# Kernel optimization log

Measured on AMD Instinct MI355X. Metric: run time of the kernel, lower is better.

Reference implementation:

```python
import jax, jax.numpy as jnp
import numpy as np

N_HEADS = 16
HEAD_DIM = 64


def apply_rope(x, cos, sin):
    # x: [B, H, S, D]; cos/sin: [S, D//2]
    x_even = x[..., ::2]
    x_odd = x[..., 1::2]
    c = cos[None, None, :, :]
    s = sin[None, None, :, :]
    rot_even = x_even * c - x_odd * s
    rot_odd = x_even * s + x_odd * c
    return jnp.stack((rot_even, rot_odd), axis=-1).reshape(x.shape)


def setup_inputs() -> dict:
    key = jax.random.key(0)
    ks = jax.random.split(key, 7)
    B, S, D = 2, 2048, 1024
    x = jax.random.normal(ks[0], (B, S, D), dtype=jnp.float32)
    # realistic rope tables
    inv_freq = 1.0 / (10000.0 ** (np.arange(0, HEAD_DIM, 2, dtype=np.float32) / HEAD_DIM))
    t = np.arange(S, dtype=np.float32)
    freqs = np.outer(t, inv_freq)  # [S, HEAD_DIM//2]
    rope_cos = jnp.asarray(np.cos(freqs), dtype=jnp.float32)
    rope_sin = jnp.asarray(np.sin(freqs), dtype=jnp.float32)
    Wqkv = jax.random.normal(ks[1], (D, 3 * D), dtype=jnp.float32) * (D ** -0.5)
    bqkv = jax.random.normal(ks[2], (3 * D,), dtype=jnp.float32) * 0.02
    Wout = jax.random.normal(ks[3], (D, D), dtype=jnp.float32) * (D ** -0.5)
    bout = jax.random.normal(ks[4], (D,), dtype=jnp.float32) * 0.02
    return {"x": x, "rope_cos": rope_cos, "rope_sin": rope_sin,
            "Wqkv": Wqkv, "bqkv": bqkv, "Wout": Wout, "bout": bout}


def reference(x, rope_cos, rope_sin, Wqkv, bqkv, Wout, bout):
    B, S, D = x.shape
    H, Hd = N_HEADS, HEAD_DIM
    qkv = x @ Wqkv + bqkv                      # [B, S, 3D]
    qkv = qkv.reshape(B, S, 3, H, Hd).transpose(2, 0, 3, 1, 4)  # [3, B, H, S, Hd]
    q, k, v = qkv[0], qkv[1], qkv[2]
    q = apply_rope(q, rope_cos, rope_sin)
    k = apply_rope(k, rope_cos, rope_sin)
    scale = Hd ** -0.5
    scores = jnp.einsum('bhqd,bhkd->bhqk', q, k) * scale
    causal = jnp.tril(jnp.ones((S, S), dtype=bool))
    scores = jnp.where(causal[None, None], scores, jnp.finfo(scores.dtype).min)
    attn = jax.nn.softmax(scores, axis=-1)
    out = jnp.einsum('bhqk,bhkd->bhqd', attn, v)  # [B, H, S, Hd]
    out = out.transpose(0, 2, 1, 3).reshape(B, S, D)
    return out @ Wout + bout
```

## Files before the change

### kernel.cpp

```cpp
#include <hip/hip_runtime.h>
#include <hip/hip_bf16.h>

typedef unsigned short u16;
typedef __attribute__((ext_vector_type(4))) float f32x4;
typedef __attribute__((ext_vector_type(16))) float f32x16;
typedef __attribute__((ext_vector_type(8))) short short8;
typedef __attribute__((ext_vector_type(8))) unsigned short ushort8;

#define AS1 __attribute__((address_space(1)))
#define AS3 __attribute__((address_space(3)))

__device__ __forceinline__ u16 f2bf(float f) {
  union { float f; unsigned u; } v; v.f = f;
  unsigned r = v.u + 0x7fffu + ((v.u >> 16) & 1u);
  return (u16)(r >> 16);
}
__device__ __forceinline__ float b2f(u16 h) {
  union { unsigned u; float f; } v; v.u = ((unsigned)h) << 16;
  return v.f;
}
__device__ __forceinline__ f32x4 mfma16(short8 a, short8 b, f32x4 c) {
  return __builtin_amdgcn_mfma_f32_16x16x32_bf16(a, b, c, 0, 0, 0);
}
__device__ __forceinline__ f32x16 mfma32(short8 a, short8 b, f32x16 c) {
  return __builtin_amdgcn_mfma_f32_32x32x16_bf16(a, b, c, 0, 0, 0);
}
__device__ __forceinline__ unsigned cvtpk(float a, float b) {
  unsigned r;
  asm("v_cvt_pk_bf16_f32 %0, %1, %2" : "=v"(r) : "v"(a), "v"(b));
  return r;
}
__device__ __forceinline__ short8 pack4(unsigned w0, unsigned w1, unsigned w2, unsigned w3) {
  union { unsigned u[4]; short8 s; } t;
  t.u[0] = w0; t.u[1] = w1; t.u[2] = w2; t.u[3] = w3;
  return t.s;
}
__device__ __forceinline__ float exp2h(float x) { return __builtin_amdgcn_exp2f(x); }

__global__ __launch_bounds__(256) void cvt_f32_bf16_k(const float* __restrict__ in,
                                                      u16* __restrict__ out, int n8) {
  int t = blockIdx.x * 256 + threadIdx.x;
  if (t >= n8) return;
  const float4* p = (const float4*)(in + (size_t)t * 8);
  float4 a = p[0], b = p[1];
  ushort8 o;
  o[0] = f2bf(a.x); o[1] = f2bf(a.y); o[2] = f2bf(a.z); o[3] = f2bf(a.w);
  o[4] = f2bf(b.x); o[5] = f2bf(b.y); o[6] = f2bf(b.z); o[7] = f2bf(b.w);
  *(ushort8*)(out + (size_t)t * 8) = o;
}

__global__ __launch_bounds__(256) void transpose_f32_bf16_k(const float* __restrict__ in,
                                                            u16* __restrict__ out, int R, int C) {
  __shared__ float tile[32][33];
  int bc = blockIdx.x * 32, br = blockIdx.y * 32;
  int tx = threadIdx.x & 31, ty = threadIdx.x >> 5;
#pragma unroll
  for (int p = 0; p < 4; ++p)
    tile[ty + p * 8][tx] = in[(size_t)(br + ty + p * 8) * C + bc + tx];
  __syncthreads();
#pragma unroll
  for (int p = 0; p < 4; ++p)
    out[(size_t)(bc + ty + p * 8) * R + br + tx] = f2bf(tile[tx][ty + p * 8]);
}

__global__ __launch_bounds__(256, 6) void gemm_n64_k(const u16* __restrict__ A,
                                                     const u16* __restrict__ Bt,
                                                     const float* __restrict__ bias,
                                                     const float* __restrict__ cosT,
                                                     const float* __restrict__ sinT,
                                                     u16* __restrict__ Cout) {
  __shared__ __align__(16) u16 As[128 * 32];
  __shared__ __align__(16) u16 Bs[64 * 32];
  const int tid = threadIdx.x, lane = tid & 63, w = tid >> 6;
  const int g = lane >> 4, c16 = lane & 15;
  const int rowBase = blockIdx.y * 128, colBase = blockIdx.x * 64;
  f32x4 acc[2][4] = {};
  const int e0 = (w * 2 + 0) * 512 + lane * 8;
  const int e1 = (w * 2 + 1) * 512 + lane * 8;
  const u16* Ag0 = A + (size_t)(rowBase + (e0 >> 5)) * 1024 + (e0 & 31);
  const u16* Ag1 = A + (size_t)(rowBase + (e1 >> 5)) * 1024 + (e1 & 31);
  const u16* Bg0 = Bt + (size_t)(colBase + (tid >> 2)) * 1024 + (tid & 3) * 8;
  u16* As0 = As + (w * 2 + 0) * 512;
  u16* As1 = As + (w * 2 + 1) * 512;
  u16* Bs0 = Bs + w * 512;

  for (int k0 = 0; k0 < 1024; k0 += 32) {
    __builtin_amdgcn_global_load_lds((const AS1 void*)(Ag0 + k0), (AS3 void*)As0, 16, 0, 0);
    __builtin_amdgcn_global_load_lds((const AS1 void*)(Ag1 + k0), (AS3 void*)As1, 16, 0, 0);
    __builtin_amdgcn_global_load_lds((const AS1 void*)(Bg0 + k0), (AS3 void*)Bs0, 16, 0, 0);
    asm volatile("s_waitcnt vmcnt(0)" ::: "memory");
    __syncthreads();
    short8 af[2], bfr[4];
#pragma unroll
    for (int i = 0; i < 2; ++i)
      af[i] = *(const short8*)(As + ((w * 32 + i * 16 + c16) * 32 + g * 8));
#pragma unroll
    for (int j = 0; j < 4; ++j)
      bfr[j] = *(const short8*)(Bs + ((j * 16 + c16) * 32 + g * 8));
#pragma unroll
    for (int i = 0; i < 2; ++i)
#pragma unroll
      for (int j = 0; j < 4; ++j) acc[i][j] = mfma16(af[i], bfr[j], acc[i][j]);
    __syncthreads();
  }

#pragma unroll
  for (int i = 0; i < 2; ++i) {
    int mbase = rowBase + w * 32 + i * 16 + 4 * g;
#pragma unroll
    for (int j = 0; j < 4; ++j) {
      int n = colBase + j * 16 + c16;
      float bv = bias[n];
      const int which = n >> 10, hh = (n >> 6) & 15, d = n & 63;
#pragma unroll
      for (int r = 0; r < 4; ++r) {
        float v = acc[i][j][r] + bv;
        int m = mbase + r;
        int bb = m >> 11, s = m & 2047;
        float outv = v;
        if (which < 2) {
          float pv = __shfl_xor(v, 1);
          float cc = cosT[(size_t)s * 32 + (d >> 1)];
          float ss = sinT[(size_t)s * 32 + (d >> 1)];
          outv = (d & 1) ? (v * cc + pv * ss) : (v * cc - pv * ss);
          if (which == 0) outv *= 0.18033688f;
        }
        Cout[((size_t)(((which * 2 + bb) * 16 + hh) * 2048 + s) << 6) + d] = f2bf(outv);
      }
    }
  }
}

__global__ __launch_bounds__(256) void gemm_out_k(const u16* __restrict__ A,
                                                  const u16* __restrict__ Bt,
                                                  const float* __restrict__ bias,
                                                  float* __restrict__ Cout) {
  __shared__ __align__(16) u16 As[128 * 32];
  __shared__ __align__(16) u16 Bs[128 * 32];
  const int tid = threadIdx.x, lane = tid & 63, w = tid >> 6;
  const int wr = w >> 1, wc = w & 1, g = lane >> 4, c16 = lane & 15;
  const int rowBase = blockIdx.y * 128, colBase = blockIdx.x * 128;
  f32x4 acc[4][4] = {};
  const int e0 = (w * 2 + 0) * 512 + lane * 8;
  const int e1 = (w * 2 + 1) * 512 + lane * 8;
  const u16* Ag0 = A + (size_t)(rowBase + (e0 >> 5)) * 1024 + (e0 & 31);
  const u16* Ag1 = A + (size_t)(rowBase + (e1 >> 5)) * 1024 + (e1 & 31);
  const u16* Bg0 = Bt + (size_t)(colBase + (e0 >> 5)) * 1024 + (e0 & 31);
  const u16* Bg1 = Bt + (size_t)(colBase + (e1 >> 5)) * 1024 + (e1 & 31);
  u16* As0 = As + (w * 2 + 0) * 512;
  u16* As1 = As + (w * 2 + 1) * 512;
  u16* Bs0 = Bs + (w * 2 + 0) * 512;
  u16* Bs1 = Bs + (w * 2 + 1) * 512;
  for (int k0 = 0; k0 < 1024; k0 += 32) {
    __builtin_amdgcn_global_load_lds((const AS1 void*)(Ag0 + k0), (AS3 void*)As0, 16, 0, 0);
    __builtin_amdgcn_global_load_lds((const AS1 void*)(Ag1 + k0), (AS3 void*)As1, 16, 0, 0);
    __builtin_amdgcn_global_load_lds((const AS1 void*)(Bg0 + k0), (AS3 void*)Bs0, 16, 0, 0);
    __builtin_amdgcn_global_load_lds((const AS1 void*)(Bg1 + k0), (AS3 void*)Bs1, 16, 0, 0);
    asm volatile("s_waitcnt vmcnt(0)" ::: "memory");
    __syncthreads();
    short8 af[4], bfr[4];
#pragma unroll
    for (int t = 0; t < 4; ++t)
      af[t] = *(const short8*)(As + ((wr * 64 + t * 16 + c16) * 32 + g * 8));
#pragma unroll
    for (int t = 0; t < 4; ++t)
      bfr[t] = *(const short8*)(Bs + ((wc * 64 + t * 16 + c16) * 32 + g * 8));
#pragma unroll
    for (int i = 0; i < 4; ++i)
#pragma unroll
      for (int j = 0; j < 4; ++j) acc[i][j] = mfma16(af[i], bfr[j], acc[i][j]);
    __syncthreads();
  }
#pragma unroll
  for (int i = 0; i < 4; ++i) {
    int mbase = rowBase + wr * 64 + i * 16 + 4 * g;
#pragma unroll
    for (int j = 0; j < 4; ++j) {
      int n = colBase + wc * 64 + j * 16 + c16;
      float bv = bias[n];
#pragma unroll
      for (int r = 0; r < 4; ++r)
        Cout[(size_t)(mbase + r) * 1024 + n] = acc[i][j][r] + bv;
    }
  }
}

__global__ __launch_bounds__(256) void vtrans_k(const u16* __restrict__ V, u16* __restrict__ Vt) {
  __shared__ u16 t[64][72];
  const int bh = blockIdx.y, s0 = blockIdx.x * 64;
  const u16* src = V + ((size_t)bh << 17);
  u16* dst = Vt + ((size_t)bh << 17);
  const int r = threadIdx.x >> 2, c0 = (threadIdx.x & 3) * 16;
  *(short8*)&t[r][c0] = *(const short8*)(src + (size_t)(s0 + r) * 64 + c0);
  *(short8*)&t[r][c0 + 8] = *(const short8*)(src + (size_t)(s0 + r) * 64 + c0 + 8);
  __syncthreads();
  const int d = threadIdx.x >> 2, sc0 = (threadIdx.x & 3) * 16;
  ushort8 o0, o1;
#pragma unroll
  for (int e = 0; e < 8; ++e) { o0[e] = t[sc0 + e][d]; o1[e] = t[sc0 + 8 + e][d]; }
  *(ushort8*)(dst + (size_t)d * 2048 + s0 + sc0) = o0;
  *(ushort8*)(dst + (size_t)d * 2048 + s0 + sc0 + 8) = o1;
}

__global__ __launch_bounds__(256, 3) void attn10_k(const u16* __restrict__ Qm,
                                                   const u16* __restrict__ Km,
                                                   const u16* __restrict__ Vtm,
                                                   u16* __restrict__ Pacc,
                                                   float* __restrict__ Ml,
                                                   u16* __restrict__ Om) {
  __shared__ __align__(16) u16 KL[2][4096];
  __shared__ __align__(16) u16 VL[2][4096];

  const int tid = threadIdx.x;
  const int lane = tid & 63, w = tid >> 6;
  const int x = blockIdx.x & 7;
  const int idx = blockIdx.x >> 3;
  const int j = idx & 3, u = idx >> 2;
  const int bh = 4 * x + j;
  int qm, t0, t1, half;
  bool split;
  if (u < 8) { qm = u; split = false; half = 0; t0 = 0; t1 = 2 * u + 2; }
  else { split = true; half = (u >= 16); qm = 15 - (u & 7); t0 = half ? (qm + 1) : 0; t1 = t0 + qm + 1; }
  const int b = bh >> 4, hd = bh & 15;
  const int qb = qm * 128 + w * 32;
  const int q32 = lane & 31, hl = lane >> 5;

  const u16* Qp = Qm + ((size_t)bh << 17);
  const u16* Kp = Km + ((size_t)bh << 17);
  const u16* Vtp = Vtm + ((size_t)bh << 17);

  const u16* qrow = Qp + ((size_t)(qb + q32) << 6) + 8 * hl;
  short8 qf[4];
#pragma unroll
  for (int ks = 0; ks < 4; ++ks) qf[ks] = *(const short8*)(qrow + 16 * ks);

  f32x16 acc0 = {}, acc1 = {};
  float m_run = -1e30f, l_run = 0.f;
  const int qg = qb + q32;
  const int rr = w * 8 + (lane >> 3);
  const int sb = (lane & 7) ^ (lane >> 3);
  const int swz = q32 & 7;

  auto stage = [&](int buf, int k0s) {
    u16* kb = &KL[buf][w * 512];
    u16* vb = &VL[buf][w * 512];
    __builtin_amdgcn_global_load_lds(
        (const AS1 void*)(Kp + ((size_t)(k0s + rr) << 6) + sb * 8),
        (AS3 void*)kb, 16, 0, 0);
    __builtin_amdgcn_global_load_lds(
        (const AS1 void*)(Kp + ((size_t)(k0s + rr + 32) << 6) + sb * 8),
        (AS3 void*)(kb + 2048), 16, 0, 0);
    __builtin_amdgcn_global_load_lds(
        (const AS1 void*)(Vtp + ((size_t)rr << 11) + k0s + sb * 8),
        (AS3 void*)vb, 16, 0, 0);
    __builtin_amdgcn_global_load_lds(
        (const AS1 void*)(Vtp + ((size_t)(rr + 32) << 11) + k0s + sb * 8),
        (AS3 void*)(vb + 2048), 16, 0, 0);
  };

  stage(0, 64 * t0);
  asm volatile("s_waitcnt vmcnt(0)" ::: "memory");
  __syncthreads();

  for (int it = t0; it < t1; ++it) {
    const int cur = (it - t0) & 1;
    if (it + 1 < t1) stage(cur ^ 1, 64 * (it + 1));
    const int k0 = 64 * it;

    if (k0 <= qb + 31) {
      const u16* Kb = &KL[cur][0];
      const u16* Vb = &VL[cur][0];

      f32x16 s0 = {}, s1 = {};
      __builtin_amdgcn_s_setprio(1);
#pragma unroll
      for (int ks = 0; ks < 4; ++ks) {
        const int cb = ((2 * ks + hl) ^ swz) * 8;
        short8 kf0 = *(const short8*)(Kb + q32 * 64 + cb);
        short8 kf1 = *(const short8*)(Kb + (32 + q32) * 64 + cb);
        s0 = mfma32(kf0, qf[ks], s0);
        s1 = mfma32(kf1, qf[ks], s1);
      }
      __builtin_amdgcn_s_setprio(0);

      short8 vfa[4], vfb[4];
#pragma unroll
      for (int ks = 0; ks < 4; ++ks) {
        const int cb = ((2 * ks + hl) ^ swz) * 8;
        vfa[ks] = *(const short8*)(Vb + q32 * 64 + cb);
        vfb[ks] = *(const short8*)(Vb + (32 + q32) * 64 + cb);
      }

      if (k0 + 63 > qb) {
#pragma unroll
        for (int r = 0; r < 16; ++r) {
          const int kvl = k0 + (r & 3) + 8 * (r >> 2) + 4 * hl;
          s0[r] = (kvl <= qg) ? s0[r] : -1e30f;
          s1[r] = (kvl + 32 <= qg) ? s1[r] : -1e30f;
        }
      }

      float pmax = s0[0];
#pragma unroll
      for (int r = 1; r < 16; ++r) pmax = fmaxf(pmax, s0[r]);
#pragma unroll
      for (int r = 0; r < 16; ++r) pmax = fmaxf(pmax, s1[r]);
      pmax = fmaxf(pmax, __shfl_xor(pmax, 32));

      if (!__all(pmax <= m_run + 11.5f)) {
        const float mn = fmaxf(m_run, pmax);
        const float alpha = exp2h(m_run - mn);
        l_run *= alpha;
        m_run = mn;
#pragma unroll
        for (int r = 0; r < 16; ++r) {
          const int row = (r & 3) + 8 * (r >> 2) + 4 * hl;
          const float ar = __shfl(alpha, row);
          acc0[r] *= ar; acc1[r] *= ar;
        }
      }

      float rs = 0.f;
#pragma unroll
      for (int r = 0; r < 16; ++r) { s0[r] = exp2h(s0[r] - m_run); rs += s0[r]; }
#pragma unroll
      for (int r = 0; r < 16; ++r) { s1[r] = exp2h(s1[r] - m_run); rs += s1[r]; }
      rs += __shfl_xor(rs, 32);
      l_run += rs;

      short8 pa[4];
#pragma unroll
      for (int t = 0; t < 2; ++t) {
        float p0, p1, p2, p3, p4, p5, p6, p7, p8, p9, pa_, pb_, pc_, pd_, pe_, pf_;
        if (t == 0) {
          p0 = s0[0];  p1 = s0[1];  p2 = s0[2];  p3 = s0[3];
          p4 = s0[4];  p5 = s0[5];  p6 = s0[6];  p7 = s0[7];
          p8 = s0[8];  p9 = s0[9];  pa_ = s0[10]; pb_ = s0[11];
          pc_ = s0[12]; pd_ = s0[13]; pe_ = s0[14]; pf_ = s0[15];
        } else {
          p0 = s1[0];  p1 = s1[1];  p2 = s1[2];  p3 = s1[3];
          p4 = s1[4];  p5 = s1[5];  p6 = s1[6];  p7 = s1[7];
          p8 = s1[8];  p9 = s1[9];  pa_ = s1[10]; pb_ = s1[11];
          pc_ = s1[12]; pd_ = s1[13]; pe_ = s1[14]; pf_ = s1[15];
        }
        const unsigned a0 = cvtpk(p0, p1), a1 = cvtpk(p2, p3);
        const unsigned a2 = cvtpk(p4, p5), a3 = cvtpk(p6, p7);
        const unsigned b0 = cvtpk(p8, p9), b1 = cvtpk(pa_, pb_);
        const unsigned b2 = cvtpk(pc_, pd_), b3 = cvtpk(pe_, pf_);
        const unsigned r0 = __shfl_xor(hl ? a0 : a2, 32);
        const unsigned r1 = __shfl_xor(hl ? a1 : a3, 32);
        pa[2 * t] = hl ? pack4(r0, r1, a2, a3) : pack4(a0, a1, r0, r1);
        const unsigned r2 = __shfl_xor(hl ? b0 : b2, 32);
        const unsigned r3 = __shfl_xor(hl ? b1 : b3, 32);
        pa[2 * t + 1] = hl ? pack4(r2, r3, b2, b3) : pack4(b0, b1, r2, r3);
      }

      __builtin_amdgcn_s_setprio(1);
#pragma unroll
      for (int ks = 0; ks < 4; ++ks) {
        acc0 = mfma32(pa[ks], vfa[ks], acc0);
        acc1 = mfma32(pa[ks], vfb[ks], acc1);
      }
      __builtin_amdgcn_s_setprio(0);
    }

    asm volatile("s_waitcnt vmcnt(0)" ::: "memory");
    __syncthreads();
  }

  if (!split) {
#pragma unroll
    for (int r = 0; r < 16; ++r) {
      const int row = (r & 3) + 8 * (r >> 2) + 4 * hl;
      const float li = 1.0f / __shfl(l_run, row);
      const int q = qb + row;
      const size_t base = ((size_t)(b * 2048 + q) << 10) + hd * 64 + q32;
      Om[base] = f2bf(acc0[r] * li);
      Om[base + 32] = f2bf(acc1[r] * li);
    }
  } else {
    const int slot = half * 256 + bh * 8 + (qm - 8);
    u16* pacc = Pacc + (size_t)slot * 8192;
#pragma unroll
    for (int r = 0; r < 16; ++r) {
      const int row = (r & 3) + 8 * (r >> 2) + 4 * hl;
      const int rl = w * 32 + row;
      pacc[rl * 64 + q32] = f2bf(acc0[r]);
      pacc[rl * 64 + q32 + 32] = f2bf(acc1[r]);
    }
    if (hl == 0) {
      Ml[(size_t)slot * 128 + w * 32 + q32] = m_run;
      Ml[65536 + (size_t)slot * 128 + w * 32 + q32] = l_run;
    }
  }
}

__global__ __launch_bounds__(256) void merge10_k(const u16* __restrict__ Pacc,
                                                 const float* __restrict__ Ml,
                                                 u16* __restrict__ Om) {
  const int x = blockIdx.x & 7;
  const int t = blockIdx.x >> 3;
  const int j = t & 3, qs = t >> 2;
  const int bh = 4 * x + j, qm = 8 + qs;
  const int b = bh >> 4, hd = bh & 15;
  const int s0 = bh * 8 + qs, s1 = 256 + s0;
  const u16* a0p = Pacc + (size_t)s0 * 8192;
  const u16* a1p = Pacc + (size_t)s1 * 8192;
#pragma unroll
  for (int k = 0; k < 4; ++k) {
    const int i = threadIdx.x + 256 * k;
    const int row = i >> 3, co = (i & 7) * 8;
    const float m0 = Ml[(size_t)s0 * 128 + row];
    const float m1 = Ml[(size_t)s1 * 128 + row];
    const float l0 = Ml[65536 + (size_t)s0 * 128 + row];
    const float l1 = Ml[65536 + (size_t)s1 * 128 + row];
    const float M = fmaxf(m0, m1);
    const float e0 = exp2h(m0 - M), e1 = exp2h(m1 - M);
    const float li = 1.0f / (l0 * e0 + l1 * e1);
    const ushort8 A0 = *(const ushort8*)(a0p + row * 64 + co);
    const ushort8 A1 = *(const ushort8*)(a1p + row * 64 + co);
    ushort8 o;
#pragma unroll
    for (int e = 0; e < 8; ++e)
      o[e] = f2bf((b2f(A0[e]) * e0 + b2f(A1[e]) * e1) * li);
    *(ushort8*)(Om + ((size_t)(b * 2048 + qm * 128 + row) << 10) + hd * 64 + co) = o;
  }
}

extern "C" void kernel_launch(void* const* d_in, const int* in_sizes, int n_in,
                              void* d_out, int out_size, void* d_ws, size_t ws_size,
                              hipStream_t stream) {
  const float* x        = (const float*)d_in[0];
  const float* rope_cos = (const float*)d_in[1];
  const float* rope_sin = (const float*)d_in[2];
  const float* Wqkv     = (const float*)d_in[3];
  const float* bqkv     = (const float*)d_in[4];
  const float* Wout     = (const float*)d_in[5];
  const float* bout     = (const float*)d_in[6];
  float* out = (float*)d_out;
  char* ws = (char*)d_ws;

  u16* Xb      = (u16*)(ws);
  u16* WqkvT   = (u16*)(ws + 8388608);
  u16* WoutT   = (u16*)(ws + 14680064);
  u16* QKV     = (u16*)(ws + 16777216);
  u16* AttnOut = (u16*)(ws + 41943040);
  u16* Vt      = (u16*)(ws + 50331648);

  u16* Pacc = (u16*)(ws);
  float* Ml = (float*)(ws + 8388608);

  cvt_f32_bf16_k<<<dim3(2048), dim3(256), 0, stream>>>(x, Xb, 524288);
  transpose_f32_bf16_k<<<dim3(96, 32), dim3(256), 0, stream>>>(Wqkv, WqkvT, 1024, 3072);
  transpose_f32_bf16_k<<<dim3(32, 32), dim3(256), 0, stream>>>(Wout, WoutT, 1024, 1024);

  gemm_n64_k<<<dim3(48, 32), dim3(256), 0, stream>>>(Xb, WqkvT, bqkv, rope_cos, rope_sin, QKV);

  u16* Qw = QKV;
  u16* Kw = QKV + (size_t)4194304;
  u16* Vw = QKV + (size_t)8388608;
  vtrans_k<<<dim3(32, 32), dim3(256), 0, stream>>>(Vw, Vt);

  attn10_k<<<dim3(768), dim3(256), 0, stream>>>(Qw, Kw, Vt, Pacc, Ml, AttnOut);
  merge10_k<<<dim3(256), dim3(256), 0, stream>>>(Pacc, Ml, AttnOut);

  gemm_out_k<<<dim3(8, 32), dim3(256), 0, stream>>>(AttnOut, WoutT, bout, out);
}
```

Before: 135.4 us.

## Pipeline QKV GEMM with 4-stage LDS ring and 128x128 tiles

Replaces the QKV projection GEMM (128x64 tiles, single-buffered, full vmcnt(0) wait each step) with a 128x128-tile kernel. It keeps a 4-deep LDS ring buffer, issuing async global-to-LDS loads two K-steps ahead and waiting only on the oldest outstanding loads. This is meant to hide global load latency and raise per-wave MFMA work and operand reuse. In exchange it uses more LDS and registers, with launch bounds lowered so fewer blocks fit per CU, and the grid halves to 768 blocks.

Measured after the change: 152.7 us. 12.7% more time.

```diff
diff --git a/kernel.cpp b/kernel.cpp
--- a/kernel.cpp
+++ b/kernel.cpp
@@ -36,6 +36,11 @@
   return t.s;
 }
 __device__ __forceinline__ float exp2h(float x) { return __builtin_amdgcn_exp2f(x); }
+
+#define WAITVM(n) do { asm volatile("s_waitcnt vmcnt(" #n ")" ::: "memory"); \
+                       __builtin_amdgcn_sched_barrier(0); } while (0)
+#define RBAR() do { __builtin_amdgcn_sched_barrier(0); __builtin_amdgcn_s_barrier(); \
+                    __builtin_amdgcn_sched_barrier(0); } while (0)
 
 __global__ __launch_bounds__(256) void cvt_f32_bf16_k(const float* __restrict__ in,
                                                       u16* __restrict__ out, int n8) {
@@ -63,53 +68,71 @@
     out[(size_t)(bc + ty + p * 8) * R + br + tx] = f2bf(tile[tx][ty + p * 8]);
 }
 
-__global__ __launch_bounds__(256, 6) void gemm_n64_k(const u16* __restrict__ A,
-                                                     const u16* __restrict__ Bt,
-                                                     const float* __restrict__ bias,
-                                                     const float* __restrict__ cosT,
-                                                     const float* __restrict__ sinT,
-                                                     u16* __restrict__ Cout) {
-  __shared__ __align__(16) u16 As[128 * 32];
-  __shared__ __align__(16) u16 Bs[64 * 32];
+__global__ __launch_bounds__(256, 2) void gemm_p_k(const u16* __restrict__ A,
+                                                   const u16* __restrict__ Bt,
+                                                   const float* __restrict__ bias,
+                                                   const float* __restrict__ cosT,
+                                                   const float* __restrict__ sinT,
+                                                   u16* __restrict__ Cout) {
+  __shared__ __align__(16) u16 As[4][4096];
+  __shared__ __align__(16) u16 Bs[4][4096];
   const int tid = threadIdx.x, lane = tid & 63, w = tid >> 6;
-  const int g = lane >> 4, c16 = lane & 15;
-  const int rowBase = blockIdx.y * 128, colBase = blockIdx.x * 64;
-  f32x4 acc[2][4] = {};
+  const int wr = w >> 1, wc = w & 1, g = lane >> 4, c16 = lane & 15;
+  const int rowBase = blockIdx.y * 128, colBase = blockIdx.x * 128;
+  f32x4 acc[4][4] = {};
   const int e0 = (w * 2 + 0) * 512 + lane * 8;
   const int e1 = (w * 2 + 1) * 512 + lane * 8;
   const u16* Ag0 = A + (size_t)(rowBase + (e0 >> 5)) * 1024 + (e0 & 31);
   const u16* Ag1 = A + (size_t)(rowBase + (e1 >> 5)) * 1024 + (e1 & 31);
-  const u16* Bg0 = Bt + (size_t)(colBase + (tid >> 2)) * 1024 + (tid & 3) * 8;
-  u16* As0 = As + (w * 2 + 0) * 512;
-  u16* As1 = As + (w * 2 + 1) * 512;
-  u16* Bs0 = Bs + w * 512;
-
-  for (int k0 = 0; k0 < 1024; k0 += 32) {
-    __builtin_amdgcn_global_load_lds((const AS1 void*)(Ag0 + k0), (AS3 void*)As0, 16, 0, 0);
-    __builtin_amdgcn_global_load_lds((const AS1 void*)(Ag1 + k0), (AS3 void*)As1, 16, 0, 0);
-    __builtin_amdgcn_global_load_lds((const AS1 void*)(Bg0 + k0), (AS3 void*)Bs0, 16, 0, 0);
-    asm volatile("s_waitcnt vmcnt(0)" ::: "memory");
-    __syncthreads();
-    short8 af[2], bfr[4];
-#pragma unroll
-    for (int i = 0; i < 2; ++i)
-      af[i] = *(const short8*)(As + ((w * 32 + i * 16 + c16) * 32 + g * 8));
-#pragma unroll
-    for (int j = 0; j < 4; ++j)
-      bfr[j] = *(const short8*)(Bs + ((j * 16 + c16) * 32 + g * 8));
-#pragma unroll
-    for (int i = 0; i < 2; ++i)
+  const u16* Bg0 = Bt + (size_t)(colBase + (e0 >> 5)) * 1024 + (e0 & 31);
+  const u16* Bg1 = Bt + (size_t)(colBase + (e1 >> 5)) * 1024 + (e1 & 31);
+  const int d0 = (w * 2 + 0) * 512;
+  const int d1 = (w * 2 + 1) * 512;
+
+  auto stage = [&](int buf, int k0) {
+    __builtin_amdgcn_global_load_lds((const AS1 void*)(Ag0 + k0), (AS3 void*)(&As[buf][d0]), 16, 0, 0);
+    __builtin_amdgcn_global_load_lds((const AS1 void*)(Ag1 + k0), (AS3 void*)(&As[buf][d1]), 16, 0, 0);
+    __builtin_amdgcn_global_load_lds((const AS1 void*)(Bg0 + k0), (AS3 void*)(&Bs[buf][d0]), 16, 0, 0);
+    __builtin_amdgcn_global_load_lds((const AS1 void*)(Bg1 + k0), (AS3 void*)(&Bs[buf][d1]), 16, 0, 0);
+  };
+  auto compute = [&](int buf) {
+    short8 af[4], bfr[4];
+#pragma unroll
+    for (int t = 0; t < 4; ++t)
+      af[t] = *(const short8*)(&As[buf][(wr * 64 + t * 16 + c16) * 32 + g * 8]);
+#pragma unroll
+    for (int t = 0; t < 4; ++t)
+      bfr[t] = *(const short8*)(&Bs[buf][(wc * 64 + t * 16 + c16) * 32 + g * 8]);
+#pragma unroll
+    for (int i = 0; i < 4; ++i)
 #pragma unroll
       for (int j = 0; j < 4; ++j) acc[i][j] = mfma16(af[i], bfr[j], acc[i][j]);
-    __syncthreads();
-  }
-
-#pragma unroll
-  for (int i = 0; i < 2; ++i) {
-    int mbase = rowBase + w * 32 + i * 16 + 4 * g;
+  };
+
+  stage(0, 0);
+  stage(1, 32);
+
+  for (int t = 0; t < 30; ++t) {
+    stage((t + 2) & 3, (t + 2) * 32);
+    WAITVM(8);
+    RBAR();
+    compute(t & 3);
+    RBAR();
+  }
+  WAITVM(4);
+  RBAR();
+  compute(30 & 3);
+  RBAR();
+  WAITVM(0);
+  RBAR();
+  compute(31 & 3);
+
+#pragma unroll
+  for (int i = 0; i < 4; ++i) {
+    int mbase = rowBase + wr * 64 + i * 16 + 4 * g;
 #pragma unroll
     for (int j = 0; j < 4; ++j) {
-      int n = colBase + j * 16 + c16;
+      int n = colBase + wc * 64 + j * 16 + c16;
       float bv = bias[n];
       const int which = n >> 10, hh = (n >> 6) & 15, d = n & 63;
 #pragma unroll
@@ -158,17 +181,17 @@
     __builtin_amdgcn_global_load_lds((const AS1 void*)(Bg1 + k0), (AS3 void*)Bs1, 16, 0, 0);
     asm volatile("s_waitcnt vmcnt(0)" ::: "memory");
     __syncthreads();
-    short8 af[4], bfr[4];
+    short8 af[4], bfr2[4];
 #pragma unroll
     for (int t = 0; t < 4; ++t)
       af[t] = *(const short8*)(As + ((wr * 64 + t * 16 + c16) * 32 + g * 8));
 #pragma unroll
     for (int t = 0; t < 4; ++t)
-      bfr[t] = *(const short8*)(Bs + ((wc * 64 + t * 16 + c16) * 32 + g * 8));
+      bfr2[t] = *(const short8*)(Bs + ((wc * 64 + t * 16 + c16) * 32 + g * 8));
 #pragma unroll
     for (int i = 0; i < 4; ++i)
 #pragma unroll
-      for (int j = 0; j < 4; ++j) acc[i][j] = mfma16(af[i], bfr[j], acc[i][j]);
+      for (int j = 0; j < 4; ++j) acc[i][j] = mfma16(af[i], bfr2[j], acc[i][j]);
     __syncthreads();
   }
 #pragma unroll
@@ -454,7 +477,7 @@
   transpose_f32_bf16_k<<<dim3(96, 32), dim3(256), 0, stream>>>(Wqkv, WqkvT, 1024, 3072);
   transpose_f32_bf16_k<<<dim3(32, 32), dim3(256), 0, stream>>>(Wout, WoutT, 1024, 1024);
 
-  gemm_n64_k<<<dim3(48, 32), dim3(256), 0, stream>>>(Xb, WqkvT, bqkv, rope_cos, rope_sin, QKV);
+  gemm_p_k<<<dim3(24, 32), dim3(256), 0, stream>>>(Xb, WqkvT, bqkv, rope_cos, rope_sin, QKV);
 
   u16* Qw = QKV;
   u16* Kw = QKV + (size_t)4194304;
```
